# Performance work log

Hardware: AMD Instinct MI355X
Metric: run time of the kernel (lower is better)

Reference implementation:

```python
import jax, jax.numpy as jnp
import numpy as np
import math

B, T, D, H = 2, 2048, 1024, 16
DH = D // H          # 64
NB = DH // 2         # 32 rope blocks
EPS = 1e-5


def _layernorm(x, g, b):
    m = jnp.mean(x, axis=-1, keepdims=True)
    v = jnp.var(x, axis=-1, keepdims=True)
    return (x - m) * jax.lax.rsqrt(v + EPS) * g + b


def _rope(x, cos, sin):
    # x: (B,H,T,DH); cos/sin: (B,H,T,NB)
    x1 = x[..., 0::2]
    x2 = x[..., 1::2]
    o1 = x1 * cos - x2 * sin
    o2 = x1 * sin + x2 * cos
    return jnp.stack([o1, o2], axis=-1).reshape(x.shape)


def setup_inputs() -> dict:
    key = jax.random.key(0)
    ks = jax.random.split(key, 16)
    x = jax.random.normal(ks[0], (B, T, D), dtype=jnp.float32)
    # genuine RoPE angles broadcast to (B,H,T,NB)
    inv_freq = 1.0 / (10000.0 ** (np.arange(NB, dtype=np.float32) / NB))
    ang = jnp.asarray(np.arange(T, dtype=np.float32)[:, None] * inv_freq[None, :])  # (T,NB)
    cos_a = jnp.broadcast_to(jnp.cos(ang)[None, None], (B, H, T, NB)).astype(jnp.float32)
    sin_a = jnp.broadcast_to(jnp.sin(ang)[None, None], (B, H, T, NB)).astype(jnp.float32)
    causal_mask = jnp.triu(jnp.ones((T, T), dtype=bool), k=1)  # True above diagonal -> masked
    s = 0.02
    def w(k, shp):
        return jax.random.normal(k, shp, dtype=jnp.float32) * s
    return {
        "x": x, "cos_a": cos_a, "sin_a": sin_a, "causal_mask": causal_mask,
        "Wq": w(ks[1], (D, D)), "bq": jnp.zeros((D,), jnp.float32),
        "Wk": w(ks[2], (D, D)), "bk": jnp.zeros((D,), jnp.float32),
        "Wv": w(ks[3], (D, D)), "bv": jnp.zeros((D,), jnp.float32),
        "Wo": w(ks[4], (D, D)), "bo": jnp.zeros((D,), jnp.float32),
        "g1": jnp.ones((D,), jnp.float32), "b1n": jnp.zeros((D,), jnp.float32),
        "g2": jnp.ones((D,), jnp.float32), "b2n": jnp.zeros((D,), jnp.float32),
        "W1": w(ks[5], (D, 4 * D)), "bf1": jnp.zeros((4 * D,), jnp.float32),
        "W2": w(ks[6], (4 * D, D)), "bf2": jnp.zeros((D,), jnp.float32),
    }


def reference(x, cos_a, sin_a, causal_mask, Wq, bq, Wk, bk, Wv, bv, Wo, bo,
              g1, b1n, g2, b2n, W1, bf1, W2, bf2):
    h = _layernorm(x, g1, b1n)
    def heads(y):
        return y.reshape(B, T, H, DH).transpose(0, 2, 1, 3)  # (B,H,T,DH)
    Q = heads(h @ Wq + bq)
    K = heads(h @ Wk + bk)
    V = heads(h @ Wv + bv)
    Q = _rope(Q, cos_a, sin_a)
    K = _rope(K, cos_a, sin_a)
    scale = math.sqrt(DH)
    scores = jnp.einsum('bhqd,bhkd->bhqk', Q, K) / scale
    scores = jnp.where(causal_mask[None, None], -jnp.inf, scores)
    attn = jax.nn.softmax(scores, axis=-1)
    out = jnp.einsum('bhqk,bhkd->bhqd', attn, V)
    out = out.transpose(0, 2, 1, 3).reshape(B, T, D)
    out = out @ Wo + bo
    x = x + out  # dropout=0.0 (eval)
    h2 = _layernorm(x, g2, b2n)
    ffn = jax.nn.gelu(h2 @ W1 + bf1, approximate=False) @ W2 + bf2
    return x + ffn
```

## Files before the change

### kernel.cpp

```cpp
#include <hip/hip_runtime.h>

typedef unsigned short u16;
typedef unsigned int   u32;
typedef __attribute__((ext_vector_type(8))) short          short8;
typedef __attribute__((ext_vector_type(4))) float          f32x4;
typedef __attribute__((ext_vector_type(8))) unsigned short u16x8;
typedef __attribute__((ext_vector_type(4))) unsigned short u16x4;

#define T_SEQ  2048
#define DMODEL 1024
#define NHEAD  16
#define DHEAD  64
#define HBUF   4194304

__device__ __forceinline__ float bf2f(u16 u) {
    u32 i = ((u32)u) << 16; float f; __builtin_memcpy(&f, &i, 4); return f;
}
__device__ __forceinline__ u16 f2bf(float f) {
    u32 x; __builtin_memcpy(&x, &f, 4);
    return (u16)((x + 0x7FFFu + ((x >> 16) & 1u)) >> 16);
}

__device__ __forceinline__ void gld16(const u16* g, u16* l) {
    auto gp = reinterpret_cast<const __attribute__((address_space(1))) u32*>(
        reinterpret_cast<uintptr_t>(g));
    auto lp = reinterpret_cast<__attribute__((address_space(3))) u32*>(
        (u32)reinterpret_cast<uintptr_t>(l));
    __builtin_amdgcn_global_load_lds(gp, lp, 16, 0, 0);
}

__global__ __launch_bounds__(256) void ln_k(const float* __restrict__ x,
                                            const float* __restrict__ g,
                                            const float* __restrict__ bb,
                                            u16* __restrict__ out)
{
    int row = blockIdx.x, tid = threadIdx.x;
    const float* xr = x + (size_t)row * DMODEL;
    f32x4 v = *(const f32x4*)(xr + tid * 4);
    float s  = v[0] + v[1] + v[2] + v[3];
    float s2 = v[0]*v[0] + v[1]*v[1] + v[2]*v[2] + v[3]*v[3];
    #pragma unroll
    for (int o = 32; o; o >>= 1) { s += __shfl_xor(s, o); s2 += __shfl_xor(s2, o); }
    __shared__ float rs[4], rq[4];
    if ((tid & 63) == 0) { rs[tid >> 6] = s; rq[tid >> 6] = s2; }
    __syncthreads();
    float S  = rs[0] + rs[1] + rs[2] + rs[3];
    float S2 = rq[0] + rq[1] + rq[2] + rq[3];
    float mean = S * (1.f / DMODEL);
    float var  = S2 * (1.f / DMODEL) - mean * mean;
    float rstd = rsqrtf(var + 1e-5f);
    f32x4 gv = *(const f32x4*)(g + tid * 4);
    f32x4 bv = *(const f32x4*)(bb + tid * 4);
    u16x4 o;
    #pragma unroll
    for (int e = 0; e < 4; e++)
        o[e] = f2bf((v[e] - mean) * rstd * gv[e] + bv[e]);
    *(u16x4*)(out + (size_t)row * DMODEL + tid * 4) = o;
}

__device__ __forceinline__ void tr_body(const float* __restrict__ in,
                                        u16* __restrict__ out, int R, int C,
                                        int bx, int by, int tid)
{
    __shared__ u16 s[64][72];
    int c0 = bx * 64, r0 = by * 64;
    #pragma unroll
    for (int p = 0; p < 2; p++) {
        int r = (tid >> 3) + p * 32, cq = (tid & 7) * 8;
        const float* ip = in + (size_t)(r0 + r) * C + c0 + cq;
        f32x4 a = *(const f32x4*)ip;
        f32x4 b = *(const f32x4*)(ip + 4);
        u16x8 o;
        #pragma unroll
        for (int e = 0; e < 4; e++) { o[e] = f2bf(a[e]); o[4 + e] = f2bf(b[e]); }
        *(u16x8*)(&s[r][cq]) = o;
    }
    __syncthreads();
    int oc = tid >> 2, kq = (tid & 3) * 16;
    u16 tmp[16] __attribute__((aligned(16)));
    #pragma unroll
    for (int e = 0; e < 16; e++) tmp[e] = s[kq + e][oc];
    u16* op = out + (size_t)(c0 + oc) * R + r0 + kq;
    *(u16x8*)op       = *(const u16x8*)(&tmp[0]);
    *(u16x8*)(op + 8) = *(const u16x8*)(&tmp[8]);
}

__global__ __launch_bounds__(256) void trall_k(const float* __restrict__ w0, const float* __restrict__ w1,
                                               const float* __restrict__ w2, const float* __restrict__ w3,
                                               const float* __restrict__ wf1, const float* __restrict__ wf2,
                                               u16* __restrict__ o0, u16* __restrict__ o1,
                                               u16* __restrict__ o2, u16* __restrict__ o3,
                                               u16* __restrict__ of1, u16* __restrict__ of2)
{
    int z = blockIdx.z;
    if (z < 4) {
        const float* in = (z == 0) ? w0 : (z == 1) ? w1 : (z == 2) ? w2 : w3;
        u16* out        = (z == 0) ? o0 : (z == 1) ? o1 : (z == 2) ? o2 : o3;
        tr_body(in, out, 1024, 1024, blockIdx.x, blockIdx.y, threadIdx.x);
    } else if (z < 8) {
        tr_body(wf1, of1, 1024, 4096, blockIdx.x + 16 * (z - 4), blockIdx.y, threadIdx.x);
    } else {
        tr_body(wf2, of2, 4096, 1024, blockIdx.x, blockIdx.y + 16 * (z - 8), threadIdx.x);
    }
}

constexpr int EPI_QKV = 0, EPI_RESF = 1, EPI_GELU = 2, EPI_RES2 = 3;

template<int EPI, int BM>
__global__ __launch_bounds__(256) void gemm_k(
    const u16* __restrict__ A, const u16* __restrict__ Bt, void* __restrict__ outv,
    int M, int N, int K, int Kld,
    const float* __restrict__ b0, const float* __restrict__ b1, const float* __restrict__ b2,
    const float* __restrict__ resid,
    const float* __restrict__ cosp, const float* __restrict__ sinp)
{
    constexpr int MI = BM / 32;
    constexpr int ASZ = BM * 32, BSZ = 128 * 32;
    __shared__ u16 As[2 * ASZ];
    __shared__ u16 Bs[2 * BSZ];
    int tid = threadIdx.x;
    int n0 = blockIdx.x * 128, m0 = blockIdx.y * BM;
    int wave = tid >> 6, lane = tid & 63, lm = lane & 15, ko = lane >> 4;
    int wm = (wave & 1) * (BM / 2), wn = (wave >> 1) * 64;
    f32x4 acc[MI][4];
    #pragma unroll
    for (int i = 0; i < MI; i++)
        #pragma unroll
        for (int j = 0; j < 4; j++) acc[i][j] = (f32x4){0.f, 0.f, 0.f, 0.f};

    int srow = wave * 16 + (lane >> 2);
    int scol = (lane & 3) * 8;
    const u16* Ag = A  + (size_t)(m0 + srow) * Kld + scol;
    const u16* Bg = Bt + (size_t)(n0 + srow) * Kld + scol;
    u16* Al = &As[wave * 16 * 32];
    u16* Bl = &Bs[wave * 16 * 32];

    gld16(Ag, Al);
    if constexpr (BM == 128) gld16(Ag + 64 * (size_t)Kld, Al + 64 * 32);
    gld16(Bg,                    Bl);
    gld16(Bg + 64 * (size_t)Kld, Bl + 64 * 32);

    int t = 0;
    for (int kt = 0; kt < K; kt += 32, t ^= 1) {
        __syncthreads();
        if (kt + 32 < K) {
            u16* Al2 = Al + (t ^ 1) * ASZ;
            u16* Bl2 = Bl + (t ^ 1) * BSZ;
            gld16(Ag + 32, Al2);
            if constexpr (BM == 128) gld16(Ag + 64 * (size_t)Kld + 32, Al2 + 64 * 32);
            gld16(Bg + 32,                    Bl2);
            gld16(Bg + 64 * (size_t)Kld + 32, Bl2 + 64 * 32);
        }
        const u16* Ab = &As[t * ASZ];
        const u16* Bb = &Bs[t * BSZ];
        short8 af[MI], bf[4];
        #pragma unroll
        for (int i = 0; i < MI; i++) af[i] = *(const short8*)(&Ab[(wm + i * 16 + lm) * 32 + ko * 8]);
        #pragma unroll
        for (int j = 0; j < 4; j++) bf[j] = *(const short8*)(&Bb[(wn + j * 16 + lm) * 32 + ko * 8]);
        #pragma unroll
        for (int i = 0; i < MI; i++)
            #pragma unroll
            for (int j = 0; j < 4; j++)
                acc[i][j] = __builtin_amdgcn_mfma_f32_16x16x32_bf16(af[i], bf[j], acc[i][j], 0, 0, 0);
        Ag += 32; Bg += 32;
    }

    #pragma unroll
    for (int i = 0; i < MI; i++) {
        #pragma unroll
        for (int j = 0; j < 4; j++) {
            int n = n0 + wn + j * 16 + lm;
            #pragma unroll
            for (int r = 0; r < 4; r++) {
                int m = m0 + wm + i * 16 + ko * 4 + r;
                float v = acc[i][j][r];
                if constexpr (EPI == EPI_QKV) {
                    int which = n >> 10, nn = n & 1023;
                    const float* bp = (which == 0) ? b0 : (which == 1 ? b1 : b2);
                    v += bp[nn];
                    float vp = __shfl_xor(v, 1);
                    int bi = m >> 11, t2 = m & 2047, hh = nn >> 6, d = nn & 63;
                    u16* outp = (u16*)outv + (size_t)which * HBUF;
                    if (which < 2) {
                        size_t oidx = ((size_t)((bi * NHEAD + hh) * T_SEQ + t2)) * DHEAD + d;
                        size_t ci = ((size_t)((bi * NHEAD + hh) * T_SEQ + t2)) * 32 + (d >> 1);
                        float c = cosp[ci], sn = sinp[ci];
                        float o = (d & 1) ? (vp * sn + v * c) : (v * c - vp * sn);
                        if (which == 0) o *= 0.18033688f;
                        outp[oidx] = f2bf(o);
                    } else {
                        size_t oidx = ((size_t)((bi * NHEAD + hh) * DHEAD + d)) * T_SEQ + t2;
                        outp[oidx] = f2bf(v);
                    }
                } else if constexpr (EPI == EPI_RESF) {
                    v += b0[n] + resid[(size_t)m * N + n];
                    ((float*)outv)[(size_t)m * N + n] = v;
                } else if constexpr (EPI == EPI_GELU) {
                    v += b0[n];
                    float gl = 0.5f * v * (1.f + erff(v * 0.70710678118654752f));
                    ((u16*)outv)[(size_t)m * N + n] = f2bf(gl);
                } else {
                    v += b0[n] + resid[(size_t)m * N + n];
                    ((float*)outv)[(size_t)m * N + n] = v;
                }
            }
        }
    }
}

__device__ __forceinline__ void attn_step(
    bool diag, int wave, int lm, int ko,
    short8 aq0, short8 aq1,
    const u16 (*sK)[72], const u16 (*sV)[72], u16 (*sPw)[72],
    f32x4* oacc, float* lr)
{
    f32x4 sacc[4];
    #pragma unroll
    for (int j = 0; j < 4; j++) {
        short8 bk0 = *(const short8*)(&sK[j * 16 + lm][ko * 8]);
        short8 bk1 = *(const short8*)(&sK[j * 16 + lm][32 + ko * 8]);
        f32x4 z = (f32x4){0.f, 0.f, 0.f, 0.f};
        z = __builtin_amdgcn_mfma_f32_16x16x32_bf16(aq0, bk0, z, 0, 0, 0);
        z = __builtin_amdgcn_mfma_f32_16x16x32_bf16(aq1, bk1, z, 0, 0, 0);
        sacc[j] = z;
    }
    if (diag) {
        #pragma unroll
        for (int j = 0; j < 4; j++)
            #pragma unroll
            for (int r = 0; r < 4; r++)
                if (j * 16 + lm > wave * 16 + ko * 4 + r) sacc[j][r] = -1e30f;
    }

    u16 pb[4][4];
    #pragma unroll
    for (int j = 0; j < 4; j++)
        #pragma unroll
        for (int r = 0; r < 4; r++) {
            float p = __builtin_amdgcn_exp2f(sacc[j][r]);
            lr[r] += p;
            pb[j][r] = f2bf(p);
        }

    #pragma unroll
    for (int j = 0; j < 4; j++)
        #pragma unroll
        for (int r = 0; r < 4; r++) sPw[ko * 4 + r][j * 16 + lm] = pb[j][r];

    #pragma unroll
    for (int ks = 0; ks < 2; ks++) {
        short8 ap = *(const short8*)(&sPw[lm][ks * 32 + ko * 8]);
        #pragma unroll
        for (int j = 0; j < 4; j++) {
            short8 bv = *(const short8*)(&sV[j * 16 + lm][ks * 32 + ko * 8]);
            oacc[j] = __builtin_amdgcn_mfma_f32_16x16x32_bf16(ap, bv, oacc[j], 0, 0, 0);
        }
    }
}

__global__ __launch_bounds__(256) void fattn_k(const u16* __restrict__ Q,
                                               const u16* __restrict__ K,
                                               const u16* __restrict__ Vt,
                                               u16* __restrict__ out)
{
    __shared__ u16 sQP[4][16][72];
    __shared__ u16 sK[2][64][72];
    __shared__ u16 sV[2][64][72];
    int tid = threadIdx.x;
    int qtA = blockIdx.x;
    int qtB = 31 - qtA;
    int bh = blockIdx.y;
    int wave = tid >> 6, lane = tid & 63, lm = lane & 15, ko = lane >> 4;
    int bi = bh >> 4, hh = bh & 15;

    const u16* Kb = K  + (size_t)bh * T_SEQ * DHEAD;
    const u16* Vb = Vt + (size_t)bh * DHEAD * T_SEQ;
    u16* sQf = &sQP[0][0][0];
    int srow = tid >> 2, scol = (tid & 3) * 16;

    short8 aqA0, aqA1, aqB0, aqB1;
    {
        const u16* QbA = Q + ((size_t)bh * T_SEQ + qtA * 64) * DHEAD + (size_t)srow * DHEAD + scol;
        *(u16x8*)(&sQf[srow * 72 + scol])     = *(const u16x8*)QbA;
        *(u16x8*)(&sQf[srow * 72 + scol + 8]) = *(const u16x8*)(QbA + 8);
        __syncthreads();
        aqA0 = *(const short8*)(&sQf[(wave * 16 + lm) * 72 + ko * 8]);
        aqA1 = *(const short8*)(&sQf[(wave * 16 + lm) * 72 + 32 + ko * 8]);
        __syncthreads();
        const u16* QbB = Q + ((size_t)bh * T_SEQ + qtB * 64) * DHEAD + (size_t)srow * DHEAD + scol;
        *(u16x8*)(&sQf[srow * 72 + scol])     = *(const u16x8*)QbB;
        *(u16x8*)(&sQf[srow * 72 + scol + 8]) = *(const u16x8*)(QbB + 8);
        __syncthreads();
        aqB0 = *(const short8*)(&sQf[(wave * 16 + lm) * 72 + ko * 8]);
        aqB1 = *(const short8*)(&sQf[(wave * 16 + lm) * 72 + 32 + ko * 8]);
    }

    f32x4 oA[4], oB[4];
    float lA[4], lB[4];
    #pragma unroll
    for (int j = 0; j < 4; j++) { oA[j] = (f32x4){0,0,0,0}; oB[j] = (f32x4){0,0,0,0}; }
    #pragma unroll
    for (int r = 0; r < 4; r++) { lA[r] = 0.f; lB[r] = 0.f; }

    int nA = qtA + 1, n = nA + qtB + 1;

    u16x8 pk0, pk1, pv0, pv1;
    {
        const u16* kp = Kb + (size_t)srow * DHEAD + scol;
        pk0 = *(const u16x8*)kp; pk1 = *(const u16x8*)(kp + 8);
        const u16* vp = Vb + (size_t)srow * T_SEQ + scol;
        pv0 = *(const u16x8*)vp; pv1 = *(const u16x8*)(vp + 8);
    }

    for (int i = 0; i < n; i++) {
        bool isA = i < nA;
        int kt = isA ? i : i - nA;
        int buf = i & 1;

        *(u16x8*)(&sK[buf][srow][scol])     = pk0;
        *(u16x8*)(&sK[buf][srow][scol + 8]) = pk1;
        *(u16x8*)(&sV[buf][srow][scol])     = pv0;
        *(u16x8*)(&sV[buf][srow][scol + 8]) = pv1;

        if (i + 1 < n) {
            int kt2 = (i + 1 < nA) ? i + 1 : i + 1 - nA;
            const u16* kp = Kb + ((size_t)(kt2 * 64 + srow)) * DHEAD + scol;
            pk0 = *(const u16x8*)kp; pk1 = *(const u16x8*)(kp + 8);
            const u16* vp = Vb + (size_t)srow * T_SEQ + kt2 * 64 + scol;
            pv0 = *(const u16x8*)vp; pv1 = *(const u16x8*)(vp + 8);
        }

        __syncthreads();

        if (isA)
            attn_step(kt == qtA, wave, lm, ko, aqA0, aqA1, sK[buf], sV[buf], sQP[wave], oA, lA);
        else
            attn_step(kt == qtB, wave, lm, ko, aqB0, aqB1, sK[buf], sV[buf], sQP[wave], oB, lB);
    }

    #pragma unroll
    for (int o = 1; o < 16; o <<= 1)
        #pragma unroll
        for (int r = 0; r < 4; r++) { lA[r] += __shfl_xor(lA[r], o); lB[r] += __shfl_xor(lB[r], o); }
    #pragma unroll
    for (int r = 0; r < 4; r++) { lA[r] = 1.f / lA[r]; lB[r] = 1.f / lB[r]; }
    int qrowA = qtA * 64 + wave * 16, qrowB = qtB * 64 + wave * 16;
    #pragma unroll
    for (int j = 0; j < 4; j++)
        #pragma unroll
        for (int r = 0; r < 4; r++) {
            out[((size_t)(bi * T_SEQ) + qrowA + ko * 4 + r) * DMODEL + hh * DHEAD + j * 16 + lm]
                = f2bf(oA[j][r] * lA[r]);
            out[((size_t)(bi * T_SEQ) + qrowB + ko * 4 + r) * DMODEL + hh * DHEAD + j * 16 + lm]
                = f2bf(oB[j][r] * lB[r]);
        }
}

extern "C" void kernel_launch(void* const* d_in, const int* in_sizes, int n_in,
                              void* d_out, int out_size, void* d_ws, size_t ws_size,
                              hipStream_t stream)
{
    (void)in_sizes; (void)n_in; (void)out_size; (void)ws_size;
    const float* x    = (const float*)d_in[0];
    const float* cosp = (const float*)d_in[1];
    const float* sinp = (const float*)d_in[2];
    const float* Wq  = (const float*)d_in[4];
    const float* bq  = (const float*)d_in[5];
    const float* Wk  = (const float*)d_in[6];
    const float* bk  = (const float*)d_in[7];
    const float* Wv  = (const float*)d_in[8];
    const float* bv  = (const float*)d_in[9];
    const float* Wo  = (const float*)d_in[10];
    const float* bo  = (const float*)d_in[11];
    const float* g1  = (const float*)d_in[12];
    const float* b1n = (const float*)d_in[13];
    const float* g2  = (const float*)d_in[14];
    const float* b2n = (const float*)d_in[15];
    const float* W1  = (const float*)d_in[16];
    const float* bf1 = (const float*)d_in[17];
    const float* W2  = (const float*)d_in[18];
    const float* bf2 = (const float*)d_in[19];

    char* ws = (char*)d_ws;
    const size_t MB = 1024 * 1024;
    u16*   qkvT  = (u16*)(ws + 0);
    u16*   WoT   = (u16*)(ws + 6 * MB);
    u16*   W1T   = (u16*)(ws + 8 * MB);
    u16*   W2T   = (u16*)(ws + 16 * MB);
    u16*   h     = (u16*)(ws + 24 * MB);
    u16*   qkvh  = (u16*)(ws + 32 * MB);
    u16*   attnC = (u16*)(ws + 56 * MB);
    float* x2    = (float*)(ws + 64 * MB);
    u16*   ffnh  = (u16*)(ws + 80 * MB);

    trall_k<<<dim3(16, 16, 12), 256, 0, stream>>>(
        Wq, Wk, Wv, Wo, W1, W2,
        qkvT, qkvT + 1 * MB, qkvT + 2 * MB, WoT, W1T, W2T);

    ln_k<<<4096, 256, 0, stream>>>(x, g1, b1n, h);
    gemm_k<EPI_QKV, 128><<<dim3(24, 32), 256, 0, stream>>>(
        h, qkvT, qkvh, 4096, 3072, 1024, 1024, bq, bk, bv, nullptr, cosp, sinp);
    fattn_k<<<dim3(16, 32), 256, 0, stream>>>(qkvh, qkvh + HBUF, qkvh + 2 * HBUF, attnC);
    gemm_k<EPI_RESF, 64><<<dim3(8, 64), 256, 0, stream>>>(
        attnC, WoT, x2, 4096, 1024, 1024, 1024, bo, nullptr, nullptr, x, nullptr, nullptr);
    ln_k<<<4096, 256, 0, stream>>>(x2, g2, b2n, h);
    gemm_k<EPI_GELU, 128><<<dim3(32, 32), 256, 0, stream>>>(
        h, W1T, ffnh, 4096, 4096, 1024, 1024, bf1, nullptr, nullptr, nullptr, nullptr, nullptr);
    gemm_k<EPI_RES2, 64><<<dim3(8, 64), 256, 0, stream>>>(
        ffnh, W2T, (float*)d_out, 4096, 1024, 4096, 4096, bf2, nullptr, nullptr, x2, nullptr, nullptr);
}
```

Measured before the change: 412.6 us.

## Triple-buffer GEMM LDS loads with explicit vmcnt waits and MFMA priority

The GEMM main loop moves from a double-buffered LDS pipeline to a three-stage ring, prefetching two K-tiles ahead. Before each barrier it waits with an explicit s_waitcnt vmcnt, so it only stalls on the tile it is about to use instead of draining every outstanding global load. It also raises wave priority around the MFMA block. The cost is 50% more LDS per block, which may lower occupancy, and the hand-written waitcnt counts and barrier placement must stay correct.

```diff
diff --git a/kernel.cpp b/kernel.cpp
--- a/kernel.cpp
+++ b/kernel.cpp
@@ -27,6 +27,12 @@
     auto lp = reinterpret_cast<__attribute__((address_space(3))) u32*>(
         (u32)reinterpret_cast<uintptr_t>(l));
     __builtin_amdgcn_global_load_lds(gp, lp, 16, 0, 0);
+}
+
+template<int N> __device__ __forceinline__ void wait_vmcnt() {
+    if constexpr (N == 0)      asm volatile("s_waitcnt vmcnt(0)" ::: "memory");
+    else if constexpr (N == 3) asm volatile("s_waitcnt vmcnt(3)" ::: "memory");
+    else                       asm volatile("s_waitcnt vmcnt(4)" ::: "memory");
 }
 
 __global__ __launch_bounds__(256) void ln_k(const float* __restrict__ x,
@@ -114,10 +120,11 @@
     const float* __restrict__ resid,
     const float* __restrict__ cosp, const float* __restrict__ sinp)
 {
-    constexpr int MI = BM / 32;
+    constexpr int MI  = BM / 32;
     constexpr int ASZ = BM * 32, BSZ = 128 * 32;
-    __shared__ u16 As[2 * ASZ];
-    __shared__ u16 Bs[2 * BSZ];
+    constexpr int G   = (BM == 128) ? 4 : 3;
+    __shared__ u16 As[3 * ASZ];
+    __shared__ u16 Bs[3 * BSZ];
     int tid = threadIdx.x;
     int n0 = blockIdx.x * 128, m0 = blockIdx.y * BM;
     int wave = tid >> 6, lane = tid & 63, lm = lane & 15, ko = lane >> 4;
@@ -135,35 +142,45 @@
     u16* Al = &As[wave * 16 * 32];
     u16* Bl = &Bs[wave * 16 * 32];
 
-    gld16(Ag, Al);
-    if constexpr (BM == 128) gld16(Ag + 64 * (size_t)Kld, Al + 64 * 32);
-    gld16(Bg,                    Bl);
-    gld16(Bg + 64 * (size_t)Kld, Bl + 64 * 32);
-
-    int t = 0;
-    for (int kt = 0; kt < K; kt += 32, t ^= 1) {
-        __syncthreads();
-        if (kt + 32 < K) {
-            u16* Al2 = Al + (t ^ 1) * ASZ;
-            u16* Bl2 = Bl + (t ^ 1) * BSZ;
-            gld16(Ag + 32, Al2);
-            if constexpr (BM == 128) gld16(Ag + 64 * (size_t)Kld + 32, Al2 + 64 * 32);
-            gld16(Bg + 32,                    Bl2);
-            gld16(Bg + 64 * (size_t)Kld + 32, Bl2 + 64 * 32);
-        }
-        const u16* Ab = &As[t * ASZ];
-        const u16* Bb = &Bs[t * BSZ];
+    auto issue = [&](int t, int b) {
+        u16* Al2 = Al + b * ASZ;
+        u16* Bl2 = Bl + b * BSZ;
+        const u16* Ag2 = Ag + t * 32;
+        const u16* Bg2 = Bg + t * 32;
+        gld16(Ag2, Al2);
+        if constexpr (BM == 128) gld16(Ag2 + 64 * (size_t)Kld, Al2 + 64 * 32);
+        gld16(Bg2,                    Bl2);
+        gld16(Bg2 + 64 * (size_t)Kld, Bl2 + 64 * 32);
+    };
+
+    int NT = K >> 5;
+    issue(0, 0);
+    issue(1, 1);
+
+    int bc = 0, bn = 2;
+    for (int kt = 0; kt < NT; kt++) {
+        if (kt + 1 < NT) wait_vmcnt<G>();
+        else             wait_vmcnt<0>();
+        __builtin_amdgcn_s_barrier();
+        __builtin_amdgcn_sched_barrier(0);
+        if (kt + 2 < NT) issue(kt + 2, bn);
+
+        const u16* Ab = &As[bc * ASZ];
+        const u16* Bb = &Bs[bc * BSZ];
         short8 af[MI], bf[4];
         #pragma unroll
         for (int i = 0; i < MI; i++) af[i] = *(const short8*)(&Ab[(wm + i * 16 + lm) * 32 + ko * 8]);
         #pragma unroll
         for (int j = 0; j < 4; j++) bf[j] = *(const short8*)(&Bb[(wn + j * 16 + lm) * 32 + ko * 8]);
+        __builtin_amdgcn_s_setprio(1);
         #pragma unroll
         for (int i = 0; i < MI; i++)
             #pragma unroll
             for (int j = 0; j < 4; j++)
                 acc[i][j] = __builtin_amdgcn_mfma_f32_16x16x32_bf16(af[i], bf[j], acc[i][j], 0, 0, 0);
-        Ag += 32; Bg += 32;
+        __builtin_amdgcn_s_setprio(0);
+        bc = (bc == 2) ? 0 : bc + 1;
+        bn = (bn == 2) ? 0 : bn + 1;
     }
 
     #pragma unroll
```

Result: no change. 404.8 us (-1.9%).
